# Kernel optimization log

Hardware: AMD Instinct MI355X
Metric: run time of the kernel (lower is better)

## Reference

```python
import jax, jax.numpy as jnp
import numpy as np

K = 3          # kernel size
STRIDE = 1
PAD = 1        # dilation*(K-1)//2
DIL = 1


def _bilinear_gather(x, py, px):
    """Bilinear sample x[B,C,H,W] at float coords (py,px) of shape [B,K2,Ho,Wo].
    Out-of-bounds contributions are zero (matches detectron2 DeformConv).
    Returns [B,C,K2,Ho,Wo]."""
    B, C, H, W = x.shape
    xf = x.reshape(B, C, H * W)
    y0 = jnp.floor(py)
    x0 = jnp.floor(px)
    out = jnp.zeros((B, C) + py.shape[1:], dtype=x.dtype)
    gather = jax.vmap(lambda xb, ib: xb[:, ib])  # ([C,HW],[K2,Ho,Wo])->[C,K2,Ho,Wo]
    for cy, cx in ((y0, x0), (y0, x0 + 1.0), (y0 + 1.0, x0), (y0 + 1.0, x0 + 1.0)):
        wgt = (1.0 - jnp.abs(py - cy)) * (1.0 - jnp.abs(px - cx))
        valid = (cy >= 0) & (cy <= H - 1) & (cx >= 0) & (cx <= W - 1)
        yi = jnp.clip(cy, 0, H - 1).astype(jnp.int32)
        xi = jnp.clip(cx, 0, W - 1).astype(jnp.int32)
        idx = yi * W + xi  # [B,K2,Ho,Wo]
        vals = gather(xf, idx)  # [B,C,K2,Ho,Wo]
        out = out + (wgt * valid.astype(x.dtype))[:, None] * vals
    return out


def _deform_conv(x, offset, weight):
    B, C, H, W = x.shape
    Ho = (H + 2 * PAD - (DIL * (K - 1) + 1)) // STRIDE + 1
    Wo = (W + 2 * PAD - (DIL * (K - 1) + 1)) // STRIDE + 1
    K2 = K * K
    # base sampling grid
    hs = (jnp.arange(Ho) * STRIDE - PAD).astype(x.dtype)  # [Ho]
    ws = (jnp.arange(Wo) * STRIDE - PAD).astype(x.dtype)  # [Wo]
    ky, kx = jnp.meshgrid(jnp.arange(K), jnp.arange(K), indexing='ij')
    ky = (ky.reshape(-1) * DIL).astype(x.dtype)  # [K2], row-major taps
    kx = (kx.reshape(-1) * DIL).astype(x.dtype)
    # offsets: channel 2k = dy, 2k+1 = dx for tap k
    off = offset.reshape(B, K2, 2, Ho, Wo)
    dy, dx = off[:, :, 0], off[:, :, 1]  # [B,K2,Ho,Wo]
    py = hs[None, None, :, None] + ky[None, :, None, None] + dy
    px = ws[None, None, None, :] + kx[None, :, None, None] + dx
    sampled = _bilinear_gather(x, py, px)  # [B,C,K2,Ho,Wo]
    wk = weight.reshape(weight.shape[0], C, K2)  # groups=1
    return jnp.einsum('ocK,bcKhw->bohw', wk, sampled)


def setup_inputs() -> dict:
    key = jax.random.key(0)
    k1, k2, k3 = jax.random.split(key, 3)
    B, C, H, W = 8, 256, 64, 64
    x = jax.random.normal(k1, (B, C, H, W), dtype=jnp.float32)
    offset = jax.random.normal(k2, (B, 2 * K * K, H, W), dtype=jnp.float32)
    weight = jax.random.normal(k3, (256, C, K, K), dtype=jnp.float32) * 0.02
    return {"x": x, "offset": offset, "weight": weight}


def reference(x, offset, weight):
    return _deform_conv(x, offset, weight)
```

## Files before the change

kernel.cpp:

```cpp
#include <hip/hip_runtime.h>
#include <stdint.h>


#define Bb 8
#define Cc 256
#define Hh 64
#define Ww 64
#define Pp 4096
#define Oo 256
#define NK2 9
#define NPAIR 36
#define BN 64
#define SROW 40
#define WT_BYTES (2u * 72u * 256u * 32u)

typedef __attribute__((ext_vector_type(4))) float f32x4;
typedef __attribute__((ext_vector_type(8))) short s16x8;
typedef __attribute__((ext_vector_type(4))) int   i32x4;

static __device__ __forceinline__ unsigned short f2bf(float f) {
    union { float f; uint32_t u; } v; v.f = f;
    return (unsigned short)((v.u + 0x7fffu + ((v.u >> 16) & 1u)) >> 16);
}
static __device__ __forceinline__ int imin(int a, int b) { return a < b ? a : b; }
static __device__ __forceinline__ int imax(int a, int b) { return a > b ? a : b; }

__global__ __launch_bounds__(256)
void prep(const float* __restrict__ x, const float* __restrict__ w,
          unsigned short* __restrict__ xt, unsigned short* __restrict__ wt) {
    __shared__ __align__(16) unsigned short L[9216];
    const int bx = blockIdx.x, tid = threadIdx.x;

    if (bx < 2048) {
        unsigned short (*t2)[72] = (unsigned short(*)[72])L;
        const int b = bx & 7, ti = bx >> 3;
        const int c0 = (ti & 3) * 64, p0 = (ti >> 2) * 64;
        #pragma unroll
        for (int rd = 0; rd < 4; rd++) {
            int c = (tid >> 4) + rd * 16;
            int px4 = (tid & 15) * 4;
            f32x4 fv = *(const f32x4*)&x[(size_t)(b * Cc + c0 + c) * Pp + p0 + px4];
            #pragma unroll
            for (int j = 0; j < 4; j++) {
                int px = px4 + j;
                int chunk = ((c >> 3) + px) & 7;
                t2[px][chunk * 8 + (c & 7)] = f2bf(fv[j]);
            }
        }
        __syncthreads();
        #pragma unroll
        for (int rd = 0; rd < 2; rd++) {
            int px = (tid >> 3) + rd * 32;
            int k = tid & 7;
            int chunk = (k + px) & 7;
            uint4 u = *(const uint4*)&t2[px][chunk * 8];
            *(uint4*)&xt[(size_t)(b * Pp + p0 + px) * Cc + c0 + k * 8] = u;
        }
    } else {
        const int o0 = (bx - 2048) * 4;
        #pragma unroll
        for (int r9 = 0; r9 < 9; r9++) {
            int idx = r9 * 256 + tid;
            f32x4 fv = *(const f32x4*)&w[(size_t)o0 * 2304 + (size_t)idx * 4];
            #pragma unroll
            for (int j = 0; j < 4; j++) L[idx * 4 + j] = f2bf(fv[j]);
        }
        __syncthreads();
        #pragma unroll 4
        for (int i = 0; i < 36; i++) {
            int ks = i * 2 + (tid >> 7);
            int r = (tid >> 5) & 3, c32 = tid & 31;
            int c = (ks & 7) * 32 + c32, k2 = ks >> 3;
            wt[(size_t)ks * 8192 + (o0 + r) * 32 + c32] = L[r * 2304 + c * 9 + k2];
        }
    }
}

__global__ __launch_bounds__(512, 4)
void dcn_main(const float* __restrict__ off, const unsigned short* __restrict__ wt,
              const unsigned short* __restrict__ xt, float* __restrict__ out) {
    __shared__ __align__(16) unsigned short Sl[2][2][BN][SROW];
    __shared__ __align__(16) int   tidx[NK2][BN][4];
    __shared__ __align__(16) float twgt[NK2][BN][4];

    const int b   = blockIdx.x & 7;
    const int p0  = (blockIdx.x >> 3) * BN;
    const int tid = threadIdx.x;
    const int lane = tid & 63;
    const int wv   = tid >> 6;
    const int quad = lane >> 4;
    const int l16  = lane & 15;
    const int moff = wv * 32;

    const int px  = tid >> 3;
    const int sub = tid & 7;
    const int hh_ = sub >> 2;
    const int cc_ = (sub & 3) * 8;

    const char* xtb = (const char*)xt + (size_t)b * Pp * Cc * 2;

    for (int t = tid; t < NK2 * BN; t += 512) {
        int k2 = t >> 6, pxl = t & 63;
        int pl = p0 + pxl;
        int hh = pl >> 6, ww = pl & 63;
        int ky = k2 / 3, kx = k2 - ky * 3;
        float dy = off[((size_t)(b * 18 + 2 * k2    ) * Pp) + pl];
        float dx = off[((size_t)(b * 18 + 2 * k2 + 1) * Pp) + pl];
        float py  = (float)(hh - 1 + ky) + dy;
        float pxf = (float)(ww - 1 + kx) + dx;
        float y0f = floorf(py), x0f = floorf(pxf);
        int   y0 = (int)y0f,  x0 = (int)x0f;
        int   y1 = y0 + 1,    x1 = x0 + 1;
        float ly = py - y0f,  lx = pxf - x0f;
        float oy = 1.f - ly,  ox = 1.f - lx;
        bool vy0 = (y0 >= 0) && (y0 < Hh);
        bool vy1 = (y1 >= 0) && (y1 < Hh);
        bool vx0 = (x0 >= 0) && (x0 < Ww);
        bool vx1 = (x1 >= 0) && (x1 < Ww);
        int cy0 = imin(imax(y0, 0), Hh - 1), cy1 = imin(imax(y1, 0), Hh - 1);
        int cx0 = imin(imax(x0, 0), Ww - 1), cx1 = imin(imax(x1, 0), Ww - 1);
        tidx[k2][pxl][0] = (cy0 * Ww + cx0) * 512;  twgt[k2][pxl][0] = (vy0 && vx0) ? oy * ox : 0.f;
        tidx[k2][pxl][1] = (cy0 * Ww + cx1) * 512;  twgt[k2][pxl][1] = (vy0 && vx1) ? oy * lx : 0.f;
        tidx[k2][pxl][2] = (cy1 * Ww + cx0) * 512;  twgt[k2][pxl][2] = (vy1 && vx0) ? ly * ox : 0.f;
        tidx[k2][pxl][3] = (cy1 * Ww + cx1) * 512;  twgt[k2][pxl][3] = (vy1 && vx1) ? ly * lx : 0.f;
    }
    __syncthreads();

    int   tio[4];
    float twv[4];
    uint4 g[4];
    {
        i32x4 ti = *(const i32x4*)&tidx[0][px][0];
        f32x4 tw = *(const f32x4*)&twgt[0][px][0];
        #pragma unroll
        for (int t = 0; t < 4; t++) { tio[t] = ti[t]; twv[t] = tw[t]; }
    }

    f32x4 acc[2][4];
    #pragma unroll
    for (int mt = 0; mt < 2; mt++)
        #pragma unroll
        for (int nt = 0; nt < 4; nt++) acc[mt][nt] = (f32x4){0.f, 0.f, 0.f, 0.f};

    auto reduce_store = [&](int prn) {
        float s0 = 0.f, s1 = 0.f, s2 = 0.f, s3 = 0.f, s4 = 0.f, s5 = 0.f, s6 = 0.f, s7 = 0.f;
        #pragma unroll
        for (int t = 0; t < 4; t++) {
            uint4 v = g[t];
            float wg = twv[t];
            s0 += wg * __uint_as_float(v.x << 16);
            s1 += wg * __uint_as_float(v.x);
            s2 += wg * __uint_as_float(v.y << 16);
            s3 += wg * __uint_as_float(v.y);
            s4 += wg * __uint_as_float(v.z << 16);
            s5 += wg * __uint_as_float(v.z);
            s6 += wg * __uint_as_float(v.w << 16);
            s7 += wg * __uint_as_float(v.w);
        }
        uint4 d;
        d.x = __builtin_amdgcn_perm(__float_as_uint(s1), __float_as_uint(s0), 0x07060302u);
        d.y = __builtin_amdgcn_perm(__float_as_uint(s3), __float_as_uint(s2), 0x07060302u);
        d.z = __builtin_amdgcn_perm(__float_as_uint(s5), __float_as_uint(s4), 0x07060302u);
        d.w = __builtin_amdgcn_perm(__float_as_uint(s7), __float_as_uint(s6), 0x07060302u);
        *(uint4*)&Sl[prn & 1][hh_][px][cc_] = d;
    };

    s16x8 afA[2][2], afB[2][2];

    auto step = [&](int pr, s16x8 (&cur)[2][2], s16x8 (&nxt)[2][2]) {
        __syncthreads();
        const int prn = pr + 1;
        if (prn < NPAIR) {
            if ((prn & 3) == 0) {
                int k2 = prn >> 2;
                i32x4 ti = *(const i32x4*)&tidx[k2][px][0];
                f32x4 tw = *(const f32x4*)&twgt[k2][px][0];
                #pragma unroll
                for (int t = 0; t < 4; t++) { tio[t] = ti[t]; twv[t] = tw[t]; }
            }
            const int coff = (prn & 3) * 128 + sub * 16;
            #pragma unroll
            for (int t = 0; t < 4; t++)
                g[t] = *(const uint4*)(xtb + tio[t] + coff);
            const char* wb = (const char*)wt + ((size_t)prn << 15);
            #pragma unroll
            for (int h = 0; h < 2; h++)
                #pragma unroll
                for (int mt = 0; mt < 2; mt++)
                    nxt[h][mt] = *(const s16x8*)(wb + h * 16384 +
                                                 (moff + mt * 16 + l16) * 64 + quad * 16);
        }
        s16x8 bfr[2][4];
        const char* sb = (const char*)&Sl[pr & 1][0][0][0];
        #pragma unroll
        for (int h = 0; h < 2; h++)
            #pragma unroll
            for (int nt = 0; nt < 4; nt++)
                bfr[h][nt] = *(const s16x8*)(sb + h * (BN * SROW * 2) +
                                             (nt * 16 + l16) * (SROW * 2) + quad * 16);
        #pragma unroll
        for (int h = 0; h < 2; h++)
            #pragma unroll
            for (int mt = 0; mt < 2; mt++)
                #pragma unroll
                for (int nt = 0; nt < 4; nt++)
                    acc[mt][nt] = __builtin_amdgcn_mfma_f32_16x16x32_bf16(
                        cur[h][mt], bfr[h][nt], acc[mt][nt], 0, 0, 0);
        if (prn < NPAIR) reduce_store(prn);
    };

    {
        #pragma unroll
        for (int t = 0; t < 4; t++)
            g[t] = *(const uint4*)(xtb + tio[t] + sub * 16);
        const char* wb = (const char*)wt;
        #pragma unroll
        for (int h = 0; h < 2; h++)
            #pragma unroll
            for (int mt = 0; mt < 2; mt++)
                afA[h][mt] = *(const s16x8*)(wb + h * 16384 +
                                             (moff + mt * 16 + l16) * 64 + quad * 16);
        reduce_store(0);
    }

    for (int pr = 0; pr < NPAIR; pr += 2) {
        step(pr,     afA, afB);
        step(pr + 1, afB, afA);
    }

    float* op = out + ((size_t)b * Oo) * Pp + p0;
    #pragma unroll
    for (int mt = 0; mt < 2; mt++)
        #pragma unroll
        for (int nt = 0; nt < 4; nt++)
            #pragma unroll
            for (int r = 0; r < 4; r++) {
                int o_ = moff + mt * 16 + quad * 4 + r;
                int p_ = nt * 16 + l16;
                op[(size_t)o_ * Pp + p_] = acc[mt][nt][r];
            }
}

extern "C" void kernel_launch(void* const* d_in, const int* in_sizes, int n_in,
                              void* d_out, int out_size, void* d_ws, size_t ws_size,
                              hipStream_t stream) {
    (void)in_sizes; (void)n_in; (void)out_size; (void)ws_size;
    const float* x   = (const float*)d_in[0];
    const float* off = (const float*)d_in[1];
    const float* w   = (const float*)d_in[2];
    float* out = (float*)d_out;

    unsigned short* wt = (unsigned short*)d_ws;
    unsigned short* xt = (unsigned short*)((char*)d_ws + WT_BYTES);

    hipLaunchKernelGGL(prep, dim3(2112), dim3(256), 0, stream, x, w, xt, wt);
    hipLaunchKernelGGL(dcn_main, dim3(512), dim3(512), 0, stream, off, wt, xt, out);
}
```

Measured before the change: 148.8 us.

## Split the kernel-tap reduction across two blocks with atomic output accumulation

```diff
diff --git a/kernel.cpp b/kernel.cpp
--- a/kernel.cpp
+++ b/kernel.cpp
@@ -10,6 +10,7 @@
 #define Oo 256
 #define NK2 9
 #define NPAIR 36
+#define HPAIR 18
 #define BN 64
 #define SROW 40
 #define WT_BYTES (2u * 72u * 256u * 32u)
@@ -83,8 +84,12 @@
     __shared__ __align__(16) int   tidx[NK2][BN][4];
     __shared__ __align__(16) float twgt[NK2][BN][4];
 
-    const int b   = blockIdx.x & 7;
-    const int p0  = (blockIdx.x >> 3) * BN;
+    const int b    = blockIdx.x & 7;
+    const int kh   = (blockIdx.x >> 3) & 1;
+    const int p0   = (blockIdx.x >> 4) * BN;
+    const int pr0  = kh * HPAIR;
+    const int prE  = pr0 + HPAIR;
+    const int k2lo = pr0 >> 2;
     const int tid = threadIdx.x;
     const int lane = tid & 63;
     const int wv   = tid >> 6;
@@ -99,8 +104,8 @@
 
     const char* xtb = (const char*)xt + (size_t)b * Pp * Cc * 2;
 
-    for (int t = tid; t < NK2 * BN; t += 512) {
-        int k2 = t >> 6, pxl = t & 63;
+    for (int t = tid; t < 5 * BN; t += 512) {
+        int k2 = (t >> 6) + k2lo, pxl = t & 63;
         int pl = p0 + pxl;
         int hh = pl >> 6, ww = pl & 63;
         int ky = k2 / 3, kx = k2 - ky * 3;
@@ -119,10 +124,13 @@
         bool vx1 = (x1 >= 0) && (x1 < Ww);
         int cy0 = imin(imax(y0, 0), Hh - 1), cy1 = imin(imax(y1, 0), Hh - 1);
         int cx0 = imin(imax(x0, 0), Ww - 1), cx1 = imin(imax(x1, 0), Ww - 1);
-        tidx[k2][pxl][0] = (cy0 * Ww + cx0) * 512;  twgt[k2][pxl][0] = (vy0 && vx0) ? oy * ox : 0.f;
-        tidx[k2][pxl][1] = (cy0 * Ww + cx1) * 512;  twgt[k2][pxl][1] = (vy0 && vx1) ? oy * lx : 0.f;
-        tidx[k2][pxl][2] = (cy1 * Ww + cx0) * 512;  twgt[k2][pxl][2] = (vy1 && vx0) ? ly * ox : 0.f;
-        tidx[k2][pxl][3] = (cy1 * Ww + cx1) * 512;  twgt[k2][pxl][3] = (vy1 && vx1) ? ly * lx : 0.f;
+        i32x4 ti; f32x4 tw;
+        ti[0] = (cy0 * Ww + cx0) * 512;  tw[0] = (vy0 && vx0) ? oy * ox : 0.f;
+        ti[1] = (cy0 * Ww + cx1) * 512;  tw[1] = (vy0 && vx1) ? oy * lx : 0.f;
+        ti[2] = (cy1 * Ww + cx0) * 512;  tw[2] = (vy1 && vx0) ? ly * ox : 0.f;
+        ti[3] = (cy1 * Ww + cx1) * 512;  tw[3] = (vy1 && vx1) ? ly * lx : 0.f;
+        *(i32x4*)&tidx[k2][pxl][0] = ti;
+        *(f32x4*)&twgt[k2][pxl][0] = tw;
     }
     __syncthreads();
 
@@ -130,8 +138,8 @@
     float twv[4];
     uint4 g[4];
     {
-        i32x4 ti = *(const i32x4*)&tidx[0][px][0];
-        f32x4 tw = *(const f32x4*)&twgt[0][px][0];
+        i32x4 ti = *(const i32x4*)&tidx[k2lo][px][0];
+        f32x4 tw = *(const f32x4*)&twgt[k2lo][px][0];
         #pragma unroll
         for (int t = 0; t < 4; t++) { tio[t] = ti[t]; twv[t] = tw[t]; }
     }
@@ -170,7 +178,7 @@
     auto step = [&](int pr, s16x8 (&cur)[2][2], s16x8 (&nxt)[2][2]) {
         __syncthreads();
         const int prn = pr + 1;
-        if (prn < NPAIR) {
+        if (prn < prE) {
             if ((prn & 3) == 0) {
                 int k2 = prn >> 2;
                 i32x4 ti = *(const i32x4*)&tidx[k2][px][0];
@@ -206,24 +214,25 @@
                 for (int nt = 0; nt < 4; nt++)
                     acc[mt][nt] = __builtin_amdgcn_mfma_f32_16x16x32_bf16(
                         cur[h][mt], bfr[h][nt], acc[mt][nt], 0, 0, 0);
-        if (prn < NPAIR) reduce_store(prn);
+        if (prn < prE) reduce_store(prn);
     };
 
     {
+        const int coff = (pr0 & 3) * 128 + sub * 16;
         #pragma unroll
         for (int t = 0; t < 4; t++)
-            g[t] = *(const uint4*)(xtb + tio[t] + sub * 16);
-        const char* wb = (const char*)wt;
+            g[t] = *(const uint4*)(xtb + tio[t] + coff);
+        const char* wb = (const char*)wt + ((size_t)pr0 << 15);
         #pragma unroll
         for (int h = 0; h < 2; h++)
             #pragma unroll
             for (int mt = 0; mt < 2; mt++)
                 afA[h][mt] = *(const s16x8*)(wb + h * 16384 +
                                              (moff + mt * 16 + l16) * 64 + quad * 16);
-        reduce_store(0);
-    }
-
-    for (int pr = 0; pr < NPAIR; pr += 2) {
+        reduce_store(pr0);
+    }
+
+    for (int pr = pr0; pr < prE; pr += 2) {
         step(pr,     afA, afB);
         step(pr + 1, afB, afA);
     }
@@ -237,14 +246,14 @@
             for (int r = 0; r < 4; r++) {
                 int o_ = moff + mt * 16 + quad * 4 + r;
                 int p_ = nt * 16 + l16;
-                op[(size_t)o_ * Pp + p_] = acc[mt][nt][r];
+                unsafeAtomicAdd(&op[(size_t)o_ * Pp + p_], acc[mt][nt][r]);
             }
 }
 
 extern "C" void kernel_launch(void* const* d_in, const int* in_sizes, int n_in,
                               void* d_out, int out_size, void* d_ws, size_t ws_size,
                               hipStream_t stream) {
-    (void)in_sizes; (void)n_in; (void)out_size; (void)ws_size;
+    (void)in_sizes; (void)n_in; (void)ws_size;
     const float* x   = (const float*)d_in[0];
     const float* off = (const float*)d_in[1];
     const float* w   = (const float*)d_in[2];
@@ -253,6 +262,7 @@
     unsigned short* wt = (unsigned short*)d_ws;
     unsigned short* xt = (unsigned short*)((char*)d_ws + WT_BYTES);
 
+    hipMemsetAsync(d_out, 0, (size_t)out_size, stream);
     hipLaunchKernelGGL(prep, dim3(2112), dim3(256), 0, stream, x, w, xt, wt);
-    hipLaunchKernelGGL(dcn_main, dim3(512), dim3(512), 0, stream, off, wt, xt, out);
-}
+    hipLaunchKernelGGL(dcn_main, dim3(1024), dim3(512), 0, stream, off, wt, xt, out);
+}
```

New measurement: 191.0 us. +28.3%, slower.
